# Optimization experiments

Hardware: AMD Instinct MI355X
Metric: run time of the kernel (lower is better)

The kernel has to match this reference:

```python
import jax, jax.numpy as jnp
import numpy as np
from jax import lax

K = 256  # top-k channels selected


def setup_inputs() -> dict:
    key = jax.random.key(0)
    k1, k2 = jax.random.split(key)
    x = jax.random.normal(k1, (32, 512, 56, 56), dtype=jnp.float32)
    w = jax.random.normal(k2, (1, 1, 3), dtype=jnp.float32)  # Conv1d(1,1,3,bias=False) weight
    return {"x": x, "w": w}


def _conv1d_channels(s, w):
    # s: [B, C] channel descriptor; conv1d over channel axis, 1 in/out channel, pad=1
    return lax.conv_general_dilated(s[:, None, :], w, window_strides=(1,), padding=[(1, 1)])[:, 0, :]


def reference(x, w):
    # x: [B, C, H, W]
    avg = jnp.mean(x, axis=(2, 3))  # [B, C]  (AdaptiveAvgPool2d((1,1)))
    mx = jnp.max(x, axis=(2, 3))    # [B, C]  (AdaptiveMaxPool2d((1,1)))
    # shared conv1d applied to both descriptors, then sum + sigmoid
    scores = jax.nn.sigmoid(_conv1d_channels(avg, w) + _conv1d_channels(mx, w))  # [B, C]
    # top-k channels per sample (values sorted descending, like torch.topk)
    vals, idx = lax.top_k(scores, K)  # [B, K] each
    # re-sort selected channels by ascending channel index (argsort of indices)
    order = jnp.argsort(idx, axis=1)
    sidx = jnp.take_along_axis(idx, order, axis=1)   # [B, K]
    svals = jnp.take_along_axis(vals, order, axis=1)  # [B, K]
    # gather selected channels from the full spatial tensor and scale
    gathered = jnp.take_along_axis(x, sidx[:, :, None, None], axis=1)  # [B, K, H, W]
    return svals[:, :, None, None] * gathered
```

## Files before the change

kernel.cpp:

```cpp
#include <hip/hip_runtime.h>
#include <math.h>

#define HW   3136
#define NC   512
#define NB   32
#define KSEL 256

typedef float f32x4 __attribute__((ext_vector_type(4)));

__global__ __launch_bounds__(256) void reduce_mean_max(
    const float* __restrict__ x, float* __restrict__ avg, float* __restrict__ mx)
{
    const int gwave = (blockIdx.x * blockDim.x + threadIdx.x) >> 6;
    const int lane  = threadIdx.x & 63;

    const f32x4* p = (const f32x4*)(x + (size_t)gwave * HW);

    float s = 0.0f;
    float m = -INFINITY;
#pragma unroll
    for (int i = 0; i < 12; ++i) {
        f32x4 v = p[lane + i * 64];
        s += (v.x + v.y) + (v.z + v.w);
        m = fmaxf(m, fmaxf(fmaxf(v.x, v.y), fmaxf(v.z, v.w)));
    }
    if (lane < 16) {
        f32x4 v = p[lane + 768];
        s += (v.x + v.y) + (v.z + v.w);
        m = fmaxf(m, fmaxf(fmaxf(v.x, v.y), fmaxf(v.z, v.w)));
    }
#pragma unroll
    for (int off = 32; off > 0; off >>= 1) {
        s += __shfl_down(s, off, 64);
        m = fmaxf(m, __shfl_down(m, off, 64));
    }
    if (lane == 0) {
        avg[gwave] = s * (1.0f / (float)HW);
        mx[gwave]  = m;
    }
}

__global__ __launch_bounds__(512) void score_topk(
    const float* __restrict__ avg, const float* __restrict__ mx,
    const float* __restrict__ w, int* __restrict__ sidx, float* __restrict__ sval)
{
    const int b = blockIdx.x;
    const int c = threadIdx.x;

    __shared__ float s_d[NC + 2];
    __shared__ float s_score[NC];
    __shared__ int   s_wcnt[8];

    if (c == 0) { s_d[0] = 0.0f; s_d[NC + 1] = 0.0f; }
    s_d[c + 1] = avg[b * NC + c] + mx[b * NC + c];
    __syncthreads();

    const float w0 = w[0], w1 = w[1], w2 = w[2];
    const float t = s_d[c] * w0 + s_d[c + 1] * w1 + s_d[c + 2] * w2;
    const float score = 1.0f / (1.0f + expf(-t));
    s_score[c] = score;
    __syncthreads();

    int rank = 0;
    for (int j = 0; j < NC; ++j) {
        const float sj = s_score[j];
        rank += (sj > score) || (sj == score && j < c);
    }
    const int flag = (rank < KSEL) ? 1 : 0;

    const unsigned long long bal = __ballot(flag);
    const int wid  = c >> 6;
    const int lane = c & 63;
    if (lane == 0) s_wcnt[wid] = __popcll(bal);
    __syncthreads();

    if (flag) {
        int pos = __popcll(bal & ((1ULL << lane) - 1ULL));
        for (int wj = 0; wj < wid; ++wj) pos += s_wcnt[wj];
        sidx[b * KSEL + pos] = c;
        sval[b * KSEL + pos] = score;
    }
}

__global__ __launch_bounds__(256) void gather_scale(
    const float* __restrict__ x, const int* __restrict__ sidx,
    const float* __restrict__ sval, float* __restrict__ out)
{
    const int bk = blockIdx.x;
    const int b  = bk >> 8;
    const int ch = sidx[bk];
    const float sv = sval[bk];

    const f32x4* src = (const f32x4*)(x + ((size_t)b * NC + ch) * HW);
    f32x4*       dst = (f32x4*)(out + (size_t)bk * HW);

    const int t = threadIdx.x;
#pragma unroll
    for (int i = 0; i < 3; ++i) {
        f32x4 v = src[t + i * 256];
        v.x *= sv; v.y *= sv; v.z *= sv; v.w *= sv;
        __builtin_nontemporal_store(v, &dst[t + i * 256]);
    }
    if (t < 16) {
        f32x4 v = src[t + 768];
        v.x *= sv; v.y *= sv; v.z *= sv; v.w *= sv;
        __builtin_nontemporal_store(v, &dst[t + 768]);
    }
}

extern "C" void kernel_launch(void* const* d_in, const int* in_sizes, int n_in,
                              void* d_out, int out_size, void* d_ws, size_t ws_size,
                              hipStream_t stream)
{
    const float* x = (const float*)d_in[0];
    const float* w = (const float*)d_in[1];
    float* out = (float*)d_out;

    float* avg  = (float*)d_ws;
    float* mx   = avg + NB * NC;
    float* sval = mx + NB * NC;
    int*   sidx = (int*)(sval + NB * KSEL);

    reduce_mean_max<<<(NB * NC) / 4, 256, 0, stream>>>(x, avg, mx);

    score_topk<<<NB, NC, 0, stream>>>(avg, mx, w, sidx, sval);

    gather_scale<<<NB * KSEL, 256, 0, stream>>>(x, sidx, sval, out);
}
```

Before: 80.73 us.

## Fuse reduce, top-k and gather into one cooperative grid-synced kernel

Replaces the three-kernel sequence with a single cooperative kernel of 256 blocks that computes channel descriptors, grid-syncs, runs per-sample scoring and top-k selection, grid-syncs again, then gathers and scales selected channels. It also stores avg+max as one combined descriptor instead of two arrays. The aim is to remove inter-kernel launch gaps. It trades this for a much smaller grid with sequential per-wave row loops, which may reduce memory-level parallelism, and it keeps the original kernels as a fallback if the cooperative launch fails.

Result: slower. 134.4 us (+66.4%).

```diff
diff --git a/kernel.cpp b/kernel.cpp
--- a/kernel.cpp
+++ b/kernel.cpp
@@ -1,23 +1,123 @@
 #include <hip/hip_runtime.h>
+#include <hip/hip_cooperative_groups.h>
 #include <math.h>
+
+namespace cg = cooperative_groups;
 
 #define HW   3136
 #define NC   512
 #define NB   32
 #define KSEL 256
+#define NBLK 256
+#define NTHR 512
 
 typedef float f32x4 __attribute__((ext_vector_type(4)));
 
+__global__ __launch_bounds__(NTHR, 2) void fused_attention(
+    const float* __restrict__ x, const float* __restrict__ w,
+    float* __restrict__ out, float* __restrict__ desc,
+    int* __restrict__ sidx, float* __restrict__ sval)
+{
+    cg::grid_group grid = cg::this_grid();
+    const int tid  = threadIdx.x;
+    const int wid  = tid >> 6;
+    const int lane = tid & 63;
+
+    {
+        const int row0 = blockIdx.x * 64;
+        for (int r = 0; r < 8; ++r) {
+            const int row = row0 + wid * 8 + r;
+            const f32x4* p = (const f32x4*)(x + (size_t)row * HW);
+            float s = 0.0f, m = -INFINITY;
+#pragma unroll
+            for (int i = 0; i < 12; ++i) {
+                f32x4 v = p[lane + i * 64];
+                s += (v.x + v.y) + (v.z + v.w);
+                m = fmaxf(m, fmaxf(fmaxf(v.x, v.y), fmaxf(v.z, v.w)));
+            }
+            if (lane < 16) {
+                f32x4 v = p[lane + 768];
+                s += (v.x + v.y) + (v.z + v.w);
+                m = fmaxf(m, fmaxf(fmaxf(v.x, v.y), fmaxf(v.z, v.w)));
+            }
+#pragma unroll
+            for (int off = 32; off; off >>= 1) {
+                s += __shfl_down(s, off, 64);
+                m = fmaxf(m, __shfl_down(m, off, 64));
+            }
+            if (lane == 0) desc[row] = s * (1.0f / (float)HW) + m;
+        }
+    }
+
+    grid.sync();
+
+    __shared__ float s_d[NC + 2];
+    __shared__ float s_score[NC];
+    __shared__ int   s_wcnt[8];
+    if (blockIdx.x < NB) {
+        const int b = blockIdx.x;
+        const int c = tid;
+        if (c == 0) { s_d[0] = 0.0f; s_d[NC + 1] = 0.0f; }
+        s_d[c + 1] = desc[b * NC + c];
+        __syncthreads();
+
+        const float w0 = w[0], w1 = w[1], w2 = w[2];
+        const float t = s_d[c] * w0 + s_d[c + 1] * w1 + s_d[c + 2] * w2;
+        const float score = 1.0f / (1.0f + expf(-t));
+        s_score[c] = score;
+        __syncthreads();
+
+        int rank = 0;
+        for (int j = 0; j < NC; ++j) {
+            const float sj = s_score[j];
+            rank += (sj > score) || (sj == score && j < c);
+        }
+        const int flag = (rank < KSEL) ? 1 : 0;
+
+        const unsigned long long bal = __ballot(flag);
+        if (lane == 0) s_wcnt[wid] = __popcll(bal);
+        __syncthreads();
+
+        if (flag) {
+            int pos = __popcll(bal & ((1ULL << lane) - 1ULL));
+            for (int wj = 0; wj < wid; ++wj) pos += s_wcnt[wj];
+            sidx[b * KSEL + pos] = c;
+            sval[b * KSEL + pos] = score;
+        }
+    }
+
+    grid.sync();
+
+    {
+        const int t = tid;
+        for (int p = 0; p < 32; ++p) {
+            const int bk = blockIdx.x * 32 + p;
+            const int b  = bk >> 8;
+            const int ch = sidx[bk];
+            const float sv = sval[bk];
+
+            const f32x4* src = (const f32x4*)(x + ((size_t)b * NC + ch) * HW);
+            f32x4*       dst = (f32x4*)(out + (size_t)bk * HW);
+
+            f32x4 v = src[t];
+            v.x *= sv; v.y *= sv; v.z *= sv; v.w *= sv;
+            __builtin_nontemporal_store(v, &dst[t]);
+            if (t < 272) {
+                f32x4 u = src[512 + t];
+                u.x *= sv; u.y *= sv; u.z *= sv; u.w *= sv;
+                __builtin_nontemporal_store(u, &dst[512 + t]);
+            }
+        }
+    }
+}
+
 __global__ __launch_bounds__(256) void reduce_mean_max(
-    const float* __restrict__ x, float* __restrict__ avg, float* __restrict__ mx)
+    const float* __restrict__ x, float* __restrict__ desc)
 {
     const int gwave = (blockIdx.x * blockDim.x + threadIdx.x) >> 6;
     const int lane  = threadIdx.x & 63;
-
     const f32x4* p = (const f32x4*)(x + (size_t)gwave * HW);
-
-    float s = 0.0f;
-    float m = -INFINITY;
+    float s = 0.0f, m = -INFINITY;
 #pragma unroll
     for (int i = 0; i < 12; ++i) {
         f32x4 v = p[lane + i * 64];
@@ -30,50 +130,40 @@
         m = fmaxf(m, fmaxf(fmaxf(v.x, v.y), fmaxf(v.z, v.w)));
     }
 #pragma unroll
-    for (int off = 32; off > 0; off >>= 1) {
+    for (int off = 32; off; off >>= 1) {
         s += __shfl_down(s, off, 64);
         m = fmaxf(m, __shfl_down(m, off, 64));
     }
-    if (lane == 0) {
-        avg[gwave] = s * (1.0f / (float)HW);
-        mx[gwave]  = m;
-    }
+    if (lane == 0) desc[gwave] = s * (1.0f / (float)HW) + m;
 }
 
 __global__ __launch_bounds__(512) void score_topk(
-    const float* __restrict__ avg, const float* __restrict__ mx,
-    const float* __restrict__ w, int* __restrict__ sidx, float* __restrict__ sval)
+    const float* __restrict__ desc, const float* __restrict__ w,
+    int* __restrict__ sidx, float* __restrict__ sval)
 {
     const int b = blockIdx.x;
     const int c = threadIdx.x;
-
     __shared__ float s_d[NC + 2];
     __shared__ float s_score[NC];
     __shared__ int   s_wcnt[8];
-
     if (c == 0) { s_d[0] = 0.0f; s_d[NC + 1] = 0.0f; }
-    s_d[c + 1] = avg[b * NC + c] + mx[b * NC + c];
+    s_d[c + 1] = desc[b * NC + c];
     __syncthreads();
-
     const float w0 = w[0], w1 = w[1], w2 = w[2];
     const float t = s_d[c] * w0 + s_d[c + 1] * w1 + s_d[c + 2] * w2;
     const float score = 1.0f / (1.0f + expf(-t));
     s_score[c] = score;
     __syncthreads();
-
     int rank = 0;
     for (int j = 0; j < NC; ++j) {
         const float sj = s_score[j];
         rank += (sj > score) || (sj == score && j < c);
     }
     const int flag = (rank < KSEL) ? 1 : 0;
-
     const unsigned long long bal = __ballot(flag);
-    const int wid  = c >> 6;
-    const int lane = c & 63;
+    const int wid = c >> 6, lane = c & 63;
     if (lane == 0) s_wcnt[wid] = __popcll(bal);
     __syncthreads();
-
     if (flag) {
         int pos = __popcll(bal & ((1ULL << lane) - 1ULL));
         for (int wj = 0; wj < wid; ++wj) pos += s_wcnt[wj];
@@ -90,10 +180,8 @@
     const int b  = bk >> 8;
     const int ch = sidx[bk];
     const float sv = sval[bk];
-
     const f32x4* src = (const f32x4*)(x + ((size_t)b * NC + ch) * HW);
     f32x4*       dst = (f32x4*)(out + (size_t)bk * HW);
-
     const int t = threadIdx.x;
 #pragma unroll
     for (int i = 0; i < 3; ++i) {
@@ -116,14 +204,17 @@
     const float* w = (const float*)d_in[1];
     float* out = (float*)d_out;
 
-    float* avg  = (float*)d_ws;
-    float* mx   = avg + NB * NC;
-    float* sval = mx + NB * NC;
+    float* desc = (float*)d_ws;
+    float* sval = desc + NB * NC;
     int*   sidx = (int*)(sval + NB * KSEL);
 
-    reduce_mean_max<<<(NB * NC) / 4, 256, 0, stream>>>(x, avg, mx);
-
-    score_topk<<<NB, NC, 0, stream>>>(avg, mx, w, sidx, sval);
-
-    gather_scale<<<NB * KSEL, 256, 0, stream>>>(x, sidx, sval, out);
-}
+    void* args[] = { (void*)&x, (void*)&w, (void*)&out,
+                     (void*)&desc, (void*)&sidx, (void*)&sval };
+    hipError_t err = hipLaunchCooperativeKernel((const void*)fused_attention,
+                                                dim3(NBLK), dim3(NTHR), args, 0, stream);
+    if (err != hipSuccess) {
+        reduce_mean_max<<<(NB * NC) / 4, 256, 0, stream>>>(x, desc);
+        score_topk<<<NB, NC, 0, stream>>>(desc, w, sidx, sval);
+        gather_scale<<<NB * KSEL, 256, 0, stream>>>(x, sidx, sval, out);
+    }
+}
```

## Fuse channel reduction and top-k selection via last-block-done atomic counter

Applied to the files above, without the earlier changes.

Merges the mean/max reduction kernel and the score/top-k kernel into one launch. Each block reduces four channel rows and stores avg+max as a single descriptor, then bumps a per-batch atomic counter; the last of the 128 blocks for a batch computes the conv, sigmoid and rank-based top-k with 256 threads handling two channels each. This removes one kernel launch and the serialized small top-k kernel, but adds a memset launch, atomics, and a tail where a single block per batch does the selection.

Measured after the change: 226.4 us. 2.8x slower.

```diff
diff --git a/kernel.cpp b/kernel.cpp
--- a/kernel.cpp
+++ b/kernel.cpp
@@ -8,77 +8,102 @@
 
 typedef float f32x4 __attribute__((ext_vector_type(4)));
 
-__global__ __launch_bounds__(256) void reduce_mean_max(
-    const float* __restrict__ x, float* __restrict__ avg, float* __restrict__ mx)
+__global__ __launch_bounds__(256) void reduce_topk(
+    const float* __restrict__ x, const float* __restrict__ w,
+    float* __restrict__ desc, unsigned int* __restrict__ counters,
+    int* __restrict__ sidx, float* __restrict__ sval)
 {
-    const int gwave = (blockIdx.x * blockDim.x + threadIdx.x) >> 6;
-    const int lane  = threadIdx.x & 63;
+    const int tid  = threadIdx.x;
+    const int wid  = tid >> 6;
+    const int lane = tid & 63;
+    const int row0 = blockIdx.x * 4;
+    const int b    = row0 >> 9;
 
-    const f32x4* p = (const f32x4*)(x + (size_t)gwave * HW);
+    {
+        const int row = row0 + wid;
+        const f32x4* p = (const f32x4*)(x + (size_t)row * HW);
+        float s = 0.0f, m = -INFINITY;
+#pragma unroll
+        for (int i = 0; i < 12; ++i) {
+            f32x4 v = p[lane + i * 64];
+            s += (v.x + v.y) + (v.z + v.w);
+            m = fmaxf(m, fmaxf(fmaxf(v.x, v.y), fmaxf(v.z, v.w)));
+        }
+        if (lane < 16) {
+            f32x4 v = p[lane + 768];
+            s += (v.x + v.y) + (v.z + v.w);
+            m = fmaxf(m, fmaxf(fmaxf(v.x, v.y), fmaxf(v.z, v.w)));
+        }
+#pragma unroll
+        for (int off = 32; off; off >>= 1) {
+            s += __shfl_down(s, off, 64);
+            m = fmaxf(m, __shfl_down(m, off, 64));
+        }
+        if (lane == 0) {
+            __hip_atomic_store(&desc[row], s * (1.0f / (float)HW) + m,
+                               __ATOMIC_RELAXED, __HIP_MEMORY_SCOPE_AGENT);
+        }
+    }
 
-    float s = 0.0f;
-    float m = -INFINITY;
-#pragma unroll
-    for (int i = 0; i < 12; ++i) {
-        f32x4 v = p[lane + i * 64];
-        s += (v.x + v.y) + (v.z + v.w);
-        m = fmaxf(m, fmaxf(fmaxf(v.x, v.y), fmaxf(v.z, v.w)));
-    }
-    if (lane < 16) {
-        f32x4 v = p[lane + 768];
-        s += (v.x + v.y) + (v.z + v.w);
-        m = fmaxf(m, fmaxf(fmaxf(v.x, v.y), fmaxf(v.z, v.w)));
-    }
-#pragma unroll
-    for (int off = 32; off > 0; off >>= 1) {
-        s += __shfl_down(s, off, 64);
-        m = fmaxf(m, __shfl_down(m, off, 64));
-    }
-    if (lane == 0) {
-        avg[gwave] = s * (1.0f / (float)HW);
-        mx[gwave]  = m;
-    }
-}
+    __syncthreads();
 
-__global__ __launch_bounds__(512) void score_topk(
-    const float* __restrict__ avg, const float* __restrict__ mx,
-    const float* __restrict__ w, int* __restrict__ sidx, float* __restrict__ sval)
-{
-    const int b = blockIdx.x;
-    const int c = threadIdx.x;
+    __shared__ unsigned int s_old;
+    if (tid == 0)
+        s_old = __hip_atomic_fetch_add(&counters[b], 1u,
+                                       __ATOMIC_ACQ_REL, __HIP_MEMORY_SCOPE_AGENT);
+    __syncthreads();
+    if (s_old != 127u) return;
 
     __shared__ float s_d[NC + 2];
     __shared__ float s_score[NC];
     __shared__ int   s_wcnt[8];
 
-    if (c == 0) { s_d[0] = 0.0f; s_d[NC + 1] = 0.0f; }
-    s_d[c + 1] = avg[b * NC + c] + mx[b * NC + c];
+    if (tid == 0) { s_d[0] = 0.0f; s_d[NC + 1] = 0.0f; }
+    s_d[tid + 1]   = __hip_atomic_load(&desc[b * NC + tid],
+                                       __ATOMIC_RELAXED, __HIP_MEMORY_SCOPE_AGENT);
+    s_d[tid + 257] = __hip_atomic_load(&desc[b * NC + tid + 256],
+                                       __ATOMIC_RELAXED, __HIP_MEMORY_SCOPE_AGENT);
     __syncthreads();
 
     const float w0 = w[0], w1 = w[1], w2 = w[2];
-    const float t = s_d[c] * w0 + s_d[c + 1] * w1 + s_d[c + 2] * w2;
-    const float score = 1.0f / (1.0f + expf(-t));
-    s_score[c] = score;
+    const int c0 = tid, c1 = tid + 256;
+    const float t0 = s_d[c0] * w0 + s_d[c0 + 1] * w1 + s_d[c0 + 2] * w2;
+    const float t1 = s_d[c1] * w0 + s_d[c1 + 1] * w1 + s_d[c1 + 2] * w2;
+    const float sc0 = 1.0f / (1.0f + expf(-t0));
+    const float sc1 = 1.0f / (1.0f + expf(-t1));
+    s_score[c0] = sc0;
+    s_score[c1] = sc1;
     __syncthreads();
 
-    int rank = 0;
+    int rank0 = 0, rank1 = 0;
     for (int j = 0; j < NC; ++j) {
         const float sj = s_score[j];
-        rank += (sj > score) || (sj == score && j < c);
+        rank0 += (sj > sc0) || (sj == sc0 && j < c0);
+        rank1 += (sj > sc1) || (sj == sc1 && j < c1);
     }
-    const int flag = (rank < KSEL) ? 1 : 0;
+    const int flag0 = (rank0 < KSEL) ? 1 : 0;
+    const int flag1 = (rank1 < KSEL) ? 1 : 0;
 
-    const unsigned long long bal = __ballot(flag);
-    const int wid  = c >> 6;
-    const int lane = c & 63;
-    if (lane == 0) s_wcnt[wid] = __popcll(bal);
+    const unsigned long long bal0 = __ballot(flag0);
+    const unsigned long long bal1 = __ballot(flag1);
+    if (lane == 0) {
+        s_wcnt[wid]     = __popcll(bal0);
+        s_wcnt[wid + 4] = __popcll(bal1);
+    }
     __syncthreads();
 
-    if (flag) {
-        int pos = __popcll(bal & ((1ULL << lane) - 1ULL));
-        for (int wj = 0; wj < wid; ++wj) pos += s_wcnt[wj];
-        sidx[b * KSEL + pos] = c;
-        sval[b * KSEL + pos] = score;
+    const unsigned long long lmask = (1ULL << lane) - 1ULL;
+    if (flag0) {
+        int pos = __popcll(bal0 & lmask);
+        for (int j = 0; j < wid; ++j) pos += s_wcnt[j];
+        sidx[b * KSEL + pos] = c0;
+        sval[b * KSEL + pos] = sc0;
+    }
+    if (flag1) {
+        int pos = __popcll(bal1 & lmask);
+        for (int j = 0; j < wid + 4; ++j) pos += s_wcnt[j];
+        sidx[b * KSEL + pos] = c1;
+        sval[b * KSEL + pos] = sc1;
     }
 }
 
@@ -116,14 +141,14 @@
     const float* w = (const float*)d_in[1];
     float* out = (float*)d_out;
 
-    float* avg  = (float*)d_ws;
-    float* mx   = avg + NB * NC;
-    float* sval = mx + NB * NC;
+    float* desc = (float*)d_ws;
+    float* sval = desc + NB * NC;
     int*   sidx = (int*)(sval + NB * KSEL);
+    unsigned int* counters = (unsigned int*)(sidx + NB * KSEL);
 
-    reduce_mean_max<<<(NB * NC) / 4, 256, 0, stream>>>(x, avg, mx);
+    hipMemsetAsync(counters, 0, NB * sizeof(unsigned int), stream);
 
-    score_topk<<<NB, NC, 0, stream>>>(avg, mx, w, sidx, sval);
+    reduce_topk<<<(NB * NC) / 4, 256, 0, stream>>>(x, w, desc, counters, sidx, sval);
 
     gather_scale<<<NB * KSEL, 256, 0, stream>>>(x, sidx, sval, out);
 }
```
